# Kernel tuning notes

Measured on AMD Instinct MI355X. Metric: run time of the kernel, lower is better.

Reference implementation:

```python
import jax, jax.numpy as jnp
import numpy as np

# Config matching init_kwargs
N_SEGMENT = 8
N_GROUP = 8
K = 3            # correlation_neighbor
PAD = K // 2     # 1
BN_EPS = 1e-5


def setup_inputs() -> dict:
    key = jax.random.key(0)
    k1, k2, k3 = jax.random.split(key, 3)
    nt, c, h, w = 64, 256, 56, 56
    x = jax.random.normal(k1, (nt, c, h, w), dtype=jnp.float32)
    # Conv2d(72 -> 144, groups=8, kernel=1): weight [144, 9, 1, 1], bias [144]
    w_conv = jax.random.normal(k2, (144, 9, 1, 1), dtype=jnp.float32) * 0.1
    b_conv = jax.random.normal(k3, (144,), dtype=jnp.float32) * 0.1
    gamma = jnp.ones((c,), dtype=jnp.float32)
    beta = jnp.zeros((c,), dtype=jnp.float32)
    return {"x": x, "w_conv": w_conv, "b_conv": b_conv, "gamma": gamma, "beta": beta}


def reference(x, w_conv, b_conv, gamma, beta):
    nt, c, h, w = x.shape
    G = N_GROUP
    cg = c // G
    nt2 = nt // 2

    # ReplicationPad2d(1)
    xp = jnp.pad(x, ((0, 0), (0, 0), (PAD, PAD), (PAD, PAD)), mode="edge")
    x_even = x[::2]          # [nt2, c, h, w]
    xp_odd = xp[1::2]        # [nt2, c, h+2, w+2]

    # Cost volume: shifted multiply + per-group channel sum, 3x3 offsets
    corrs = []
    for i in range(K):
        for j in range(K):
            corr = x_even * jax.lax.slice(xp_odd, (0, 0, i, j), (nt2, c, i + h, j + w))
            corr = corr.reshape(nt2, G, cg, h, w).sum(axis=2)  # [nt2, G, h, w]
            corrs.append(corr)
    corr_feat = jnp.stack(corrs, axis=1)  # [nt2, 9, G, h, w] (offset outer, group inner)

    # Grouped 1x1 conv (groups=G): contiguous channel split of the [9*G] layout
    cr = corr_feat.reshape(nt2, G, K * K, h, w)               # [nt2, G, 9, h, w]
    wg = w_conv.reshape(G, 2 * K * K, K * K)                  # [G, 18, 9]
    xcorr = jnp.einsum("ngihw,goi->ngohw", cr, wg) + b_conv.reshape(1, G, 2 * K * K, 1, 1)
    # view(nt2, 3, 3, 2*G, h, w)
    xcorr = xcorr.reshape(nt2, K, K, 2 * G, h, w)

    # x_pad viewed as (nt, c_per_group, n_group, H+2, W+2)  (group is inner here!)
    xp2 = xp.reshape(nt, cg, G, h + 2, w + 2)
    xp_e = xp2[::2]   # even frames [nt2, cg, G, h+2, w+2]
    xp_o = xp2[1::2]  # odd frames

    # Weighted re-fusion over the 9 offsets (accumulate to avoid a big stack)
    acc = jnp.zeros((nt2, cg, G, h, w), dtype=x.dtype)
    for i in range(K):
        for j in range(K):
            we = xcorr[:, i, j, 0::2][:, None]  # [nt2, 1, G, h, w]
            wo = xcorr[:, i, j, 1::2][:, None]
            acc = acc + xp_e[:, :, :, i:i + h, j:j + w] * we \
                      + xp_o[:, :, :, i:i + h, j:j + w] * wo
    out = acc.reshape(nt2, c, h, w)  # (cg outer, G inner) flatten matches torch view

    # BatchNorm2d (training-mode batch statistics)
    mean = out.mean(axis=(0, 2, 3), keepdims=True)
    var = out.var(axis=(0, 2, 3), keepdims=True)
    out = (out - mean) * jax.lax.rsqrt(var + BN_EPS)
    out = out * gamma.reshape(1, c, 1, 1) + beta.reshape(1, c, 1, 1)
    return out
```

## Files before the change

### kernel.cpp

```cpp
#include <hip/hip_runtime.h>
#include <cstdint>

#define HW 3136
#define WID 56
#define NBLK 1792
#define RSTR 14336

typedef float f4v __attribute__((ext_vector_type(4)));

__device__ __forceinline__ int clampi(int v, int lo, int hi) {
    return v < lo ? lo : (v > hi ? hi : v);
}
__device__ __forceinline__ uint32_t rne16(float f) {
    uint32_t b = __float_as_uint(f);
    return (b + 0x7fffu + ((b >> 16) & 1u)) >> 16;
}
__device__ __forceinline__ float blo(uint32_t u) { return __uint_as_float(u << 16); }
__device__ __forceinline__ float bhi(uint32_t u) { return __uint_as_float(u & 0xffff0000u); }
__device__ __forceinline__ uint32_t bpermu(int a4, uint32_t v) {
    return (uint32_t)__builtin_amdgcn_ds_bpermute(a4, (int)v);
}
__device__ __forceinline__ float bperm(int a4, float v) {
    return __int_as_float(__builtin_amdgcn_ds_bpermute(a4, __float_as_int(v)));
}
__device__ __forceinline__ void fma2(float2& a, const float2& u, const float2& w) {
    a.x += u.x * w.x; a.y += u.y * w.y;
}

__global__ __launch_bounds__(256) void tf_pack_t(const float* __restrict__ x,
                                                 uint32_t* __restrict__ xb)
{
    const unsigned total4 = 8192u * 784u;
    unsigned i = blockIdx.x * 256u + threadIdx.x;
    const unsigned stride = gridDim.x * 256u;
    uint4* xb4 = (uint4*)xb;
    for (; i < total4; i += stride) {
        const unsigned p4 = i / 784u;
        const unsigned i4 = i - p4 * 784u;
        const unsigned pair = p4 >> 8;
        const unsigned ch = p4 & 255u;
        const unsigned row = i4 / 14u;
        const unsigned c4 = i4 - row * 14u;
        const size_t eoff = ((size_t)pair * 512 + ch) * HW + i4 * 4;
        const f4v e = __builtin_nontemporal_load((const f4v*)(x + eoff));
        const f4v o = __builtin_nontemporal_load((const f4v*)(x + eoff + (size_t)256 * HW));
        uint4 u;
        u.x = (rne16(o.x) << 16) | rne16(e.x);
        u.y = (rne16(o.y) << 16) | rne16(e.y);
        u.z = (rne16(o.z) << 16) | rne16(e.z);
        u.w = (rne16(o.w) << 16) | rne16(e.w);
        xb4[(((size_t)pair * 56 + row) * 256 + ch) * 14 + c4] = u;
    }
}

__global__ __launch_bounds__(256, 2) void tf_fused_t(
    const uint32_t* __restrict__ xb, const float* __restrict__ wconv,
    const float* __restrict__ bconv, float* __restrict__ out)
{
    __shared__ float CP[2 * 9 * 56];
    __shared__ float CR[72 * 56];

    const int d = blockIdx.x;
    const int logical = (d & 7) * 224 + (d >> 3);
    const int n  = logical / 56;
    const int r0 = logical % 56;
    const int t = threadIdx.x;
    const int su = __builtin_amdgcn_readfirstlane(t >> 6);
    const int lane = t & 63;
    const bool act = lane < WID;
    const int px = act ? lane : 55;

    const uint32_t* xq = xb + (size_t)n * 56 * RSTR;

    const int am = clampi(lane - 1, 0, 55) * 4;
    const int ap = clampi(lane + 1, 0, 55) * 4;

    const int Rm = clampi(r0 - 1, 0, 55) * RSTR;
    const int Rc = r0 * RSTR;
    const int Rp = clampi(r0 + 1, 0, 55) * RSTR;

    for (int g = 0; g < 8; ++g) {
        float crg[9];
        #pragma unroll
        for (int i = 0; i < 9; ++i) crg[i] = 0.f;

        #pragma unroll
        for (int sub = 0; sub < 4; ++sub) {
            const int ch0 = (g * 4 + sub) * 8 + 2 * su;
            #pragma unroll
            for (int c = 0; c < 2; ++c) {
                const int co = (ch0 + c) * 56 + px;
                const uint32_t u0 = xq[Rm + co];
                const uint32_t u1 = xq[Rc + co];
                const uint32_t u2 = xq[Rp + co];
                const float e = blo(u1);
                {   const uint32_t um = bpermu(am, u0), up = bpermu(ap, u0);
                    crg[0] += e * bhi(um); crg[1] += e * bhi(u0); crg[2] += e * bhi(up); }
                {   const uint32_t um = bpermu(am, u1), up = bpermu(ap, u1);
                    crg[3] += e * bhi(um); crg[4] += e * bhi(u1); crg[5] += e * bhi(up); }
                {   const uint32_t um = bpermu(am, u2), up = bpermu(ap, u2);
                    crg[6] += e * bhi(um); crg[7] += e * bhi(u2); crg[8] += e * bhi(up); }
            }
        }
        if (su < 2 && act) {
            #pragma unroll
            for (int ij = 0; ij < 9; ++ij) CP[(su * 9 + ij) * 56 + px] = crg[ij];
        }
        __syncthreads();
        if (su >= 2 && act) {
            const int sl = su - 2;
            #pragma unroll
            for (int ij = 0; ij < 9; ++ij) CP[(sl * 9 + ij) * 56 + px] += crg[ij];
        }
        __syncthreads();
        if (su == 0 && act) {
            #pragma unroll
            for (int ij = 0; ij < 9; ++ij)
                CR[(ij * 8 + g) * 56 + px] =
                    CP[(0 * 9 + ij) * 56 + px] + CP[(1 * 9 + ij) * 56 + px];
        }
        __syncthreads();
    }

    float Wv[9][4];
    #pragma unroll
    for (int ij = 0; ij < 9; ++ij)
        #pragma unroll
        for (int j = 0; j < 4; ++j) {
            const int f = ij * 16 + 4 * su + j;
            const int a = f / 18;
            float w = bconv[f];
            #pragma unroll
            for (int b = 0; b < 9; ++b)
                w += CR[(a * 9 + b) * 56 + px] * wconv[f * 9 + b];
            Wv[ij][j] = w;
        }

    float* ob = out + (size_t)n * 256 * HW + r0 * WID;

    #pragma unroll 2
    for (int q = 0; q < 32; ++q) {
        const int ch0 = q * 8 + 2 * su;
        float a0 = 0.f, a1 = 0.f;
        #pragma unroll
        for (int c = 0; c < 2; ++c) {
            const int co = (ch0 + c) * 56 + px;
            const uint32_t u0 = xq[Rm + co];
            const uint32_t u1 = xq[Rc + co];
            const uint32_t u2 = xq[Rp + co];
            float acc = 0.f;
            {   const uint32_t um = bpermu(am, u0), up = bpermu(ap, u0);
                acc += blo(um) * Wv[0][2 * c] + bhi(um) * Wv[0][2 * c + 1];
                acc += blo(u0) * Wv[1][2 * c] + bhi(u0) * Wv[1][2 * c + 1];
                acc += blo(up) * Wv[2][2 * c] + bhi(up) * Wv[2][2 * c + 1]; }
            {   const uint32_t um = bpermu(am, u1), up = bpermu(ap, u1);
                acc += blo(um) * Wv[3][2 * c] + bhi(um) * Wv[3][2 * c + 1];
                acc += blo(u1) * Wv[4][2 * c] + bhi(u1) * Wv[4][2 * c + 1];
                acc += blo(up) * Wv[5][2 * c] + bhi(up) * Wv[5][2 * c + 1]; }
            {   const uint32_t um = bpermu(am, u2), up = bpermu(ap, u2);
                acc += blo(um) * Wv[6][2 * c] + bhi(um) * Wv[6][2 * c + 1];
                acc += blo(u2) * Wv[7][2 * c] + bhi(u2) * Wv[7][2 * c + 1];
                acc += blo(up) * Wv[8][2 * c] + bhi(up) * Wv[8][2 * c + 1]; }
            if (c == 0) a0 = acc; else a1 = acc;
        }
        if (act) {
            ob[(size_t)ch0 * HW + px] = a0;
            ob[(size_t)(ch0 + 1) * HW + px] = a1;
        }
    }
}

__global__ __launch_bounds__(256, 2) void tf_fused_f32(
    const float* __restrict__ x, const float* __restrict__ wconv,
    const float* __restrict__ bconv, float* __restrict__ out)
{
    __shared__ float2 CP[2 * 9 * 28];
    __shared__ float  CR[72 * 56];

    const int d = blockIdx.x;
    const int logical = (d & 7) * 224 + (d >> 3);
    const int n  = logical / 56;
    const int r0 = logical % 56;
    const int t = threadIdx.x;
    const int wv = t >> 6;
    const int l = t & 63;
    const int sub = l >> 5;
    const int s8 = wv * 2 + sub;
    const int qd0 = l & 31;
    const bool act = qd0 < 28;
    const int qd = act ? qd0 : 27;

    const float* xe = x + (size_t)(2 * n) * 256 * HW;
    const float* xo = xe + (size_t)256 * HW;

    const int am = ((qd0 == 0) ? l : (l - 1)) * 4;
    const int ap = ((qd0 >= 27) ? l : (l + 1)) * 4;
    const bool le = (qd0 == 0);
    const bool re = (qd0 >= 27);

    int rb[3];
    #pragma unroll
    for (int di = 0; di < 3; ++di) rb[di] = clampi(r0 + di - 1, 0, 55) * WID + qd * 2;
    const int rc = r0 * WID + qd * 2;

#define MKTAPS2(v, Tm, Tp)                                  \
    {                                                       \
        const float lwp = bperm(am, (v).y);                 \
        const float rwp = bperm(ap, (v).x);                 \
        Tm = make_float2(le ? (v).x : lwp, (v).x);          \
        Tp = make_float2((v).y, re ? (v).y : rwp);          \
    }

    for (int g = 0; g < 8; ++g) {
        const int ch0 = g * 32 + 4 * s8;
        const float* pe = xe + (size_t)ch0 * HW;
        const float* po = xo + (size_t)ch0 * HW;
        float2 crg[9];
        #pragma unroll
        for (int i = 0; i < 9; ++i) crg[i] = make_float2(0.f, 0.f);
        #pragma unroll
        for (int c = 0; c < 4; ++c) {
            const float2 E = *(const float2*)(pe + (size_t)c * HW + rc);
            #pragma unroll
            for (int di = 0; di < 3; ++di) {
                const float2 O = *(const float2*)(po + (size_t)c * HW + rb[di]);
                float2 Tm, Tp;
                MKTAPS2(O, Tm, Tp)
                fma2(crg[di * 3 + 0], E, Tm);
                fma2(crg[di * 3 + 1], E, O);
                fma2(crg[di * 3 + 2], E, Tp);
            }
        }
        #pragma unroll
        for (int ij = 0; ij < 9; ++ij) {
            crg[ij].x += __shfl_xor(crg[ij].x, 32);
            crg[ij].y += __shfl_xor(crg[ij].y, 32);
        }
        if (wv < 2 && sub == 0 && act) {
            #pragma unroll
            for (int ij = 0; ij < 9; ++ij) CP[(wv * 9 + ij) * 28 + qd] = crg[ij];
        }
        __syncthreads();
        if (wv >= 2 && sub == 0 && act) {
            const int sl = wv - 2;
            #pragma unroll
            for (int ij = 0; ij < 9; ++ij) {
                float2 v = CP[(sl * 9 + ij) * 28 + qd];
                v.x += crg[ij].x; v.y += crg[ij].y;
                CP[(sl * 9 + ij) * 28 + qd] = v;
            }
        }
        __syncthreads();
        if (wv == 0 && sub == 0 && act) {
            #pragma unroll
            for (int ij = 0; ij < 9; ++ij) {
                const float2 v0 = CP[(0 * 9 + ij) * 28 + qd];
                const float2 v1 = CP[(1 * 9 + ij) * 28 + qd];
                float2 v;
                v.x = v0.x + v1.x; v.y = v0.y + v1.y;
                *(float2*)(CR + (ij * 8 + g) * 56 + qd * 2) = v;
            }
        }
        __syncthreads();
    }

    float2 We[9], Wo[9];
    #pragma unroll
    for (int ij = 0; ij < 9; ++ij) {
        const int fe = ij * 16 + 2 * s8;
        const int a = fe / 18;
        const float be = bconv[fe], bo = bconv[fe + 1];
        float2 we = make_float2(be, be);
        float2 wo = make_float2(bo, bo);
        #pragma unroll
        for (int b = 0; b < 9; ++b) {
            const float2 c2 = *(const float2*)(CR + (a * 9 + b) * 56 + qd * 2);
            const float wce = wconv[fe * 9 + b];
            const float wco = wconv[fe * 9 + 9 + b];
            we.x += c2.x * wce; we.y += c2.y * wce;
            wo.x += c2.x * wco; wo.y += c2.y * wco;
        }
        We[ij] = we; Wo[ij] = wo;
    }

    float* ob = out + (size_t)n * 256 * HW + r0 * WID + qd * 2;
    #pragma unroll 2
    for (int k = 0; k < 32; ++k) {
        const int ch = k * 8 + s8;
        const float* pe = xe + (size_t)ch * HW;
        const float* po = xo + (size_t)ch * HW;
        float2 acc = make_float2(0.f, 0.f);
        #pragma unroll
        for (int di = 0; di < 3; ++di) {
            const float2 Ev = *(const float2*)(pe + rb[di]);
            const float2 Ov = *(const float2*)(po + rb[di]);
            float2 TEm, TEp, TOm, TOp;
            MKTAPS2(Ev, TEm, TEp)
            MKTAPS2(Ov, TOm, TOp)
            fma2(acc, TEm, We[di * 3 + 0]); fma2(acc, TOm, Wo[di * 3 + 0]);
            fma2(acc, Ev,  We[di * 3 + 1]); fma2(acc, Ov,  Wo[di * 3 + 1]);
            fma2(acc, TEp, We[di * 3 + 2]); fma2(acc, TOp, Wo[di * 3 + 2]);
        }
        if (act) *(float2*)(ob + (size_t)ch * HW) = acc;
    }
#undef MKTAPS2
}

__global__ void tf_stats_part(const float* __restrict__ out,
                              float* __restrict__ ps, float* __restrict__ pq)
{
    const int ch = blockIdx.x >> 3;
    const int sl = blockIdx.x & 7;
    const int t = threadIdx.x;

    float s = 0.f, q = 0.f;
    #pragma unroll
    for (int k = 0; k < 4; ++k) {
        const float4* p = (const float4*)(out + ((size_t)(4 * sl + k) * 256 + ch) * HW);
        for (int i = t; i < 784; i += 256) {
            const float4 v = p[i];
            s += v.x + v.y + v.z + v.w;
            q += v.x * v.x + v.y * v.y + v.z * v.z + v.w * v.w;
        }
    }
    #pragma unroll
    for (int o = 32; o >= 1; o >>= 1) {
        s += __shfl_xor(s, o);
        q += __shfl_xor(q, o);
    }
    __shared__ float rs[4], rq[4];
    if ((t & 63) == 0) { rs[t >> 6] = s; rq[t >> 6] = q; }
    __syncthreads();
    if (t == 0) {
        ps[blockIdx.x] = rs[0] + rs[1] + rs[2] + rs[3];
        pq[blockIdx.x] = rq[0] + rq[1] + rq[2] + rq[3];
    }
}

__global__ void tf_stats_fin(const float* __restrict__ ps, const float* __restrict__ pq,
                             const float* __restrict__ gamma, const float* __restrict__ beta,
                             float* __restrict__ AB)
{
    const int ch = threadIdx.x;
    float s = 0.f, q = 0.f;
    #pragma unroll
    for (int sl = 0; sl < 8; ++sl) {
        s += ps[ch * 8 + sl];
        q += pq[ch * 8 + sl];
    }
    const float inv = 1.f / 100352.f;
    const float mean = s * inv;
    const float var = q * inv - mean * mean;
    const float rstd = rsqrtf(var + 1e-5f);
    const float A = gamma[ch] * rstd;
    AB[ch] = A;
    AB[256 + ch] = beta[ch] - mean * A;
}

__global__ void tf_norm(float* __restrict__ out, const float* __restrict__ AB)
{
    const unsigned total4 = 32u * 256u * 784u;
    unsigned i = blockIdx.x * 256u + threadIdx.x;
    const unsigned stride = gridDim.x * 256u;
    float4* o4 = (float4*)out;
    for (; i < total4; i += stride) {
        const unsigned ch = (i / 784u) & 255u;
        const float A = AB[ch], B = AB[256 + ch];
        float4 v = o4[i];
        v.x = v.x * A + B;
        v.y = v.y * A + B;
        v.z = v.z * A + B;
        v.w = v.w * A + B;
        o4[i] = v;
    }
}

extern "C" void kernel_launch(void* const* d_in, const int* in_sizes, int n_in,
                              void* d_out, int out_size, void* d_ws, size_t ws_size,
                              hipStream_t stream) {
    const float* x     = (const float*)d_in[0];
    const float* wconv = (const float*)d_in[1];
    const float* bconv = (const float*)d_in[2];
    const float* gamma = (const float*)d_in[3];
    const float* beta  = (const float*)d_in[4];
    float* out = (float*)d_out;

    float* ps = (float*)d_ws;
    float* pq = ps + 2048;
    float* AB = pq + 2048;
    uint32_t* xbuf = (uint32_t*)((uint8_t*)d_ws + 32768);
    const size_t need = 32768 + (size_t)32 * 56 * RSTR * 4;

    if (ws_size >= need) {
        tf_pack_t<<<4096, 256, 0, stream>>>(x, xbuf);
        tf_fused_t<<<NBLK, 256, 0, stream>>>(xbuf, wconv, bconv, out);
    } else {
        tf_fused_f32<<<NBLK, 256, 0, stream>>>(x, wconv, bconv, out);
    }
    tf_stats_part<<<2048, 256, 0, stream>>>(out, ps, pq);
    tf_stats_fin<<<1, 256, 0, stream>>>(ps, pq, gamma, beta, AB);
    tf_norm<<<2048, 256, 0, stream>>>(out, AB);
}
```

Measured before the change: 193.3 us.

## Process two pixels per lane in fused bf16 kernel with half-wave channel split

Reworks the fused kernel so each lane handles two adjacent pixels (28 lanes per row) and each half-wave handles a different channel, giving 8 channel slots per block instead of 4. Loads become 64-bit, and only the outer neighbours need cross-lane permutes, so fewer bpermute operations are issued per pixel. Half-waves are reduced with a xor shuffle before the shared-memory reduction. The output loop also prefetches the next channel's rows one iteration ahead. The cost is more registers for the float2 weights and accumulators, and a different lane-to-pixel mapping that needs special handling at the row edges.

```diff
diff --git a/kernel.cpp b/kernel.cpp
--- a/kernel.cpp
+++ b/kernel.cpp
@@ -53,120 +53,146 @@
     }
 }
 
-__global__ __launch_bounds__(256, 2) void tf_fused_t(
+__global__ __launch_bounds__(256, 2) void tf_fused_t2(
     const uint32_t* __restrict__ xb, const float* __restrict__ wconv,
     const float* __restrict__ bconv, float* __restrict__ out)
 {
-    __shared__ float CP[2 * 9 * 56];
-    __shared__ float CR[72 * 56];
+    __shared__ float2 CP[2 * 9 * 28];
+    __shared__ float  CR[72 * 56];
 
     const int d = blockIdx.x;
     const int logical = (d & 7) * 224 + (d >> 3);
     const int n  = logical / 56;
     const int r0 = logical % 56;
     const int t = threadIdx.x;
-    const int su = __builtin_amdgcn_readfirstlane(t >> 6);
-    const int lane = t & 63;
-    const bool act = lane < WID;
-    const int px = act ? lane : 55;
+    const int wv = t >> 6;
+    const int l = t & 63;
+    const int sub = l >> 5;
+    const int s8 = wv * 2 + sub;
+    const int qd0 = l & 31;
+    const bool act = qd0 < 28;
+    const int qd = act ? qd0 : 27;
 
     const uint32_t* xq = xb + (size_t)n * 56 * RSTR;
 
-    const int am = clampi(lane - 1, 0, 55) * 4;
-    const int ap = clampi(lane + 1, 0, 55) * 4;
+    const int am = ((qd0 == 0) ? l : (l - 1)) * 4;
+    const int ap = ((qd0 >= 27) ? l : (l + 1)) * 4;
+    const bool le = (qd0 == 0);
+    const bool re = (qd0 >= 27);
 
     const int Rm = clampi(r0 - 1, 0, 55) * RSTR;
     const int Rc = r0 * RSTR;
     const int Rp = clampi(r0 + 1, 0, 55) * RSTR;
+    const int co0 = qd * 2;
 
     for (int g = 0; g < 8; ++g) {
-        float crg[9];
-        #pragma unroll
-        for (int i = 0; i < 9; ++i) crg[i] = 0.f;
-
-        #pragma unroll
-        for (int sub = 0; sub < 4; ++sub) {
-            const int ch0 = (g * 4 + sub) * 8 + 2 * su;
-            #pragma unroll
-            for (int c = 0; c < 2; ++c) {
-                const int co = (ch0 + c) * 56 + px;
-                const uint32_t u0 = xq[Rm + co];
-                const uint32_t u1 = xq[Rc + co];
-                const uint32_t u2 = xq[Rp + co];
-                const float e = blo(u1);
-                {   const uint32_t um = bpermu(am, u0), up = bpermu(ap, u0);
-                    crg[0] += e * bhi(um); crg[1] += e * bhi(u0); crg[2] += e * bhi(up); }
-                {   const uint32_t um = bpermu(am, u1), up = bpermu(ap, u1);
-                    crg[3] += e * bhi(um); crg[4] += e * bhi(u1); crg[5] += e * bhi(up); }
-                {   const uint32_t um = bpermu(am, u2), up = bpermu(ap, u2);
-                    crg[6] += e * bhi(um); crg[7] += e * bhi(u2); crg[8] += e * bhi(up); }
-            }
-        }
-        if (su < 2 && act) {
-            #pragma unroll
-            for (int ij = 0; ij < 9; ++ij) CP[(su * 9 + ij) * 56 + px] = crg[ij];
-        }
-        __syncthreads();
-        if (su >= 2 && act) {
-            const int sl = su - 2;
-            #pragma unroll
-            for (int ij = 0; ij < 9; ++ij) CP[(sl * 9 + ij) * 56 + px] += crg[ij];
-        }
-        __syncthreads();
-        if (su == 0 && act) {
-            #pragma unroll
-            for (int ij = 0; ij < 9; ++ij)
-                CR[(ij * 8 + g) * 56 + px] =
-                    CP[(0 * 9 + ij) * 56 + px] + CP[(1 * 9 + ij) * 56 + px];
-        }
-        __syncthreads();
-    }
-
-    float Wv[9][4];
-    #pragma unroll
-    for (int ij = 0; ij < 9; ++ij)
-        #pragma unroll
-        for (int j = 0; j < 4; ++j) {
-            const int f = ij * 16 + 4 * su + j;
-            const int a = f / 18;
-            float w = bconv[f];
-            #pragma unroll
-            for (int b = 0; b < 9; ++b)
-                w += CR[(a * 9 + b) * 56 + px] * wconv[f * 9 + b];
-            Wv[ij][j] = w;
-        }
-
-    float* ob = out + (size_t)n * 256 * HW + r0 * WID;
+        float2 crg[9];
+        #pragma unroll
+        for (int i = 0; i < 9; ++i) crg[i] = make_float2(0.f, 0.f);
+
+        #pragma unroll
+        for (int c = 0; c < 4; ++c) {
+            const int co = (g * 32 + 4 * s8 + c) * 56 + co0;
+            const uint2 U0 = *(const uint2*)(xq + Rm + co);
+            const uint2 U1 = *(const uint2*)(xq + Rc + co);
+            const uint2 U2 = *(const uint2*)(xq + Rp + co);
+            const float e0 = blo(U1.x), e1 = blo(U1.y);
+            #pragma unroll
+            for (int r = 0; r < 3; ++r) {
+                const uint2 U = (r == 0) ? U0 : ((r == 1) ? U1 : U2);
+                uint32_t lw = bpermu(am, U.y); if (le) lw = U.x;
+                uint32_t rw = bpermu(ap, U.x); if (re) rw = U.y;
+                crg[r * 3 + 0].x += e0 * bhi(lw);
+                crg[r * 3 + 0].y += e1 * bhi(U.x);
+                crg[r * 3 + 1].x += e0 * bhi(U.x);
+                crg[r * 3 + 1].y += e1 * bhi(U.y);
+                crg[r * 3 + 2].x += e0 * bhi(U.y);
+                crg[r * 3 + 2].y += e1 * bhi(rw);
+            }
+        }
+
+        #pragma unroll
+        for (int ij = 0; ij < 9; ++ij) {
+            crg[ij].x += __shfl_xor(crg[ij].x, 32);
+            crg[ij].y += __shfl_xor(crg[ij].y, 32);
+        }
+        if (wv < 2 && sub == 0 && act) {
+            #pragma unroll
+            for (int ij = 0; ij < 9; ++ij) CP[(wv * 9 + ij) * 28 + qd] = crg[ij];
+        }
+        __syncthreads();
+        if (wv >= 2 && sub == 0 && act) {
+            const int sl = wv - 2;
+            #pragma unroll
+            for (int ij = 0; ij < 9; ++ij) {
+                float2 v = CP[(sl * 9 + ij) * 28 + qd];
+                v.x += crg[ij].x; v.y += crg[ij].y;
+                CP[(sl * 9 + ij) * 28 + qd] = v;
+            }
+        }
+        __syncthreads();
+        if (wv == 0 && sub == 0 && act) {
+            #pragma unroll
+            for (int ij = 0; ij < 9; ++ij) {
+                const float2 v0 = CP[(0 * 9 + ij) * 28 + qd];
+                const float2 v1 = CP[(1 * 9 + ij) * 28 + qd];
+                float2 v;
+                v.x = v0.x + v1.x; v.y = v0.y + v1.y;
+                *(float2*)(CR + (ij * 8 + g) * 56 + qd * 2) = v;
+            }
+        }
+        __syncthreads();
+    }
+
+    float2 We[9], Wo[9];
+    #pragma unroll
+    for (int ij = 0; ij < 9; ++ij) {
+        const int fe = ij * 16 + 2 * s8;
+        const int a = fe / 18;
+        const float be = bconv[fe], bo = bconv[fe + 1];
+        float2 we = make_float2(be, be);
+        float2 wo = make_float2(bo, bo);
+        #pragma unroll
+        for (int b = 0; b < 9; ++b) {
+            const float2 c2 = *(const float2*)(CR + (a * 9 + b) * 56 + qd * 2);
+            const float wce = wconv[fe * 9 + b];
+            const float wco = wconv[fe * 9 + 9 + b];
+            we.x += c2.x * wce; we.y += c2.y * wce;
+            wo.x += c2.x * wco; wo.y += c2.y * wco;
+        }
+        We[ij] = we; Wo[ij] = wo;
+    }
+
+    float* ob = out + (size_t)n * 256 * HW + r0 * WID + co0;
+
+    uint2 C0 = *(const uint2*)(xq + Rm + s8 * 56 + co0);
+    uint2 C1 = *(const uint2*)(xq + Rc + s8 * 56 + co0);
+    uint2 C2 = *(const uint2*)(xq + Rp + s8 * 56 + co0);
 
     #pragma unroll 2
-    for (int q = 0; q < 32; ++q) {
-        const int ch0 = q * 8 + 2 * su;
-        float a0 = 0.f, a1 = 0.f;
-        #pragma unroll
-        for (int c = 0; c < 2; ++c) {
-            const int co = (ch0 + c) * 56 + px;
-            const uint32_t u0 = xq[Rm + co];
-            const uint32_t u1 = xq[Rc + co];
-            const uint32_t u2 = xq[Rp + co];
-            float acc = 0.f;
-            {   const uint32_t um = bpermu(am, u0), up = bpermu(ap, u0);
-                acc += blo(um) * Wv[0][2 * c] + bhi(um) * Wv[0][2 * c + 1];
-                acc += blo(u0) * Wv[1][2 * c] + bhi(u0) * Wv[1][2 * c + 1];
-                acc += blo(up) * Wv[2][2 * c] + bhi(up) * Wv[2][2 * c + 1]; }
-            {   const uint32_t um = bpermu(am, u1), up = bpermu(ap, u1);
-                acc += blo(um) * Wv[3][2 * c] + bhi(um) * Wv[3][2 * c + 1];
-                acc += blo(u1) * Wv[4][2 * c] + bhi(u1) * Wv[4][2 * c + 1];
-                acc += blo(up) * Wv[5][2 * c] + bhi(up) * Wv[5][2 * c + 1]; }
-            {   const uint32_t um = bpermu(am, u2), up = bpermu(ap, u2);
-                acc += blo(um) * Wv[6][2 * c] + bhi(um) * Wv[6][2 * c + 1];
-                acc += blo(u2) * Wv[7][2 * c] + bhi(u2) * Wv[7][2 * c + 1];
-                acc += blo(up) * Wv[8][2 * c] + bhi(up) * Wv[8][2 * c + 1]; }
-            if (c == 0) a0 = acc; else a1 = acc;
-        }
-        if (act) {
-            ob[(size_t)ch0 * HW + px] = a0;
-            ob[(size_t)(ch0 + 1) * HW + px] = a1;
-        }
+    for (int k = 0; k < 32; ++k) {
+        const int kn = (k < 31) ? k + 1 : 31;
+        const int con = (kn * 8 + s8) * 56 + co0;
+        const uint2 N0 = *(const uint2*)(xq + Rm + con);
+        const uint2 N1 = *(const uint2*)(xq + Rc + con);
+        const uint2 N2 = *(const uint2*)(xq + Rp + con);
+
+        float2 acc = make_float2(0.f, 0.f);
+        #pragma unroll
+        for (int r = 0; r < 3; ++r) {
+            const uint2 U = (r == 0) ? C0 : ((r == 1) ? C1 : C2);
+            uint32_t lw = bpermu(am, U.y); if (le) lw = U.x;
+            uint32_t rw = bpermu(ap, U.x); if (re) rw = U.y;
+            acc.x += blo(lw)  * We[r * 3 + 0].x + bhi(lw)  * Wo[r * 3 + 0].x;
+            acc.y += blo(U.x) * We[r * 3 + 0].y + bhi(U.x) * Wo[r * 3 + 0].y;
+            acc.x += blo(U.x) * We[r * 3 + 1].x + bhi(U.x) * Wo[r * 3 + 1].x;
+            acc.y += blo(U.y) * We[r * 3 + 1].y + bhi(U.y) * Wo[r * 3 + 1].y;
+            acc.x += blo(U.y) * We[r * 3 + 2].x + bhi(U.y) * Wo[r * 3 + 2].x;
+            acc.y += blo(rw)  * We[r * 3 + 2].y + bhi(rw)  * Wo[r * 3 + 2].y;
+        }
+        if (act) *(float2*)(ob + (size_t)(k * 8 + s8) * HW) = acc;
+
+        C0 = N0; C1 = N1; C2 = N2;
     }
 }
 
@@ -393,7 +419,7 @@
 
     if (ws_size >= need) {
         tf_pack_t<<<4096, 256, 0, stream>>>(x, xbuf);
-        tf_fused_t<<<NBLK, 256, 0, stream>>>(xbuf, wconv, bconv, out);
+        tf_fused_t2<<<NBLK, 256, 0, stream>>>(xbuf, wconv, bconv, out);
     } else {
         tf_fused_f32<<<NBLK, 256, 0, stream>>>(x, wconv, bconv, out);
     }
```

After: 194.0 us. No clear change (+0.4%).
